# Kernel tuning notes

Hardware: AMD Instinct MI355X
Metric: run time of the kernel (lower is better)

The kernel has to match this reference:

```python
import jax, jax.numpy as jnp
import numpy as np

B, N, D = 8, 1024, 768
H, HD = 12, 64


def setup_inputs() -> dict:
    key = jax.random.key(0)
    ks = jax.random.split(key, 9)
    return {
        "x": jax.random.normal(ks[0], (B, N, D), dtype=jnp.float32),
        "Wq": jax.random.normal(ks[1], (H, HD, HD), dtype=jnp.float32) * (HD ** -0.5),
        "Wk": jax.random.normal(ks[2], (H, HD, HD), dtype=jnp.float32) * (HD ** -0.5),
        "Wv": jax.random.normal(ks[3], (H, HD, HD), dtype=jnp.float32) * (HD ** -0.5),
        "bq": jax.random.normal(ks[4], (H, HD), dtype=jnp.float32) * 0.02,
        "bk": jax.random.normal(ks[5], (H, HD), dtype=jnp.float32) * 0.02,
        "bv": jax.random.normal(ks[6], (H, HD), dtype=jnp.float32) * 0.02,
        "Wo": jax.random.normal(ks[7], (D, D), dtype=jnp.float32) * (D ** -0.5),
        "bo": jnp.zeros((D,), dtype=jnp.float32),
    }


def reference(x, Wq, Wk, Wv, bq, bk, bv, Wo, bo):
    # x: [B, N, D]; split into H heads of size HD along the feature dim
    b, n, d = x.shape
    h, hd = Wq.shape[0], Wq.shape[1]
    xh = x.reshape(b, n, h, hd)
    # per-head linear projections (stacked nn.Linear(head_dim, head_dim))
    q = jnp.einsum('bnhd,hde->bhne', xh, Wq) + bq[None, :, None, :]
    k = jnp.einsum('bnhd,hde->bhne', xh, Wk) + bk[None, :, None, :]
    v = jnp.einsum('bnhd,hde->bhne', xh, Wv) + bv[None, :, None, :]
    # NOTE: faithful quirk - scale uses FULL dim, not head_dim
    scale = d ** -0.5
    scores = jnp.einsum('bhid,bhjd->bhij', q, k) * scale  # [B,H,N,N]
    attn = jax.nn.softmax(scores, axis=-1)
    out = jnp.einsum('bhij,bhjd->bhid', attn, v)  # [B,H,N,HD]
    out = out.transpose(0, 2, 1, 3).reshape(b, n, d)  # concat heads
    return out @ Wo.T + bo  # wO: nn.Linear(dim, dim)
```

## Files before the change

kernel.cpp:

```cpp
#include <hip/hip_runtime.h>


typedef __attribute__((ext_vector_type(8))) short short8;
typedef __attribute__((ext_vector_type(4))) float floatx4;

#define MFMA16(a, b, c) __builtin_amdgcn_mfma_f32_16x16x32_bf16((a), (b), (c), 0, 0, 0)

#if __has_builtin(__builtin_amdgcn_exp2f)
#define EXP2(x) __builtin_amdgcn_exp2f(x)
#else
#define EXP2(x) __expf(0.6931471805599453f * (x))
#endif
#if __has_builtin(__builtin_amdgcn_rcpf)
#define RCP(x) __builtin_amdgcn_rcpf(x)
#else
#define RCP(x) (1.0f / (x))
#endif

__device__ __forceinline__ unsigned short f2bf(float f) {
    union { float f; unsigned int i; } c;
    c.f = f;
    unsigned int i = c.i;
    return (unsigned short)((i + 0x7fffu + ((i >> 16) & 1u)) >> 16);
}
__device__ __forceinline__ unsigned short f2bf_trunc(float f) {
    union { float f; unsigned int i; } c;
    c.f = f;
    return (unsigned short)(c.i >> 16);
}

__global__ __launch_bounds__(256) void prep_weights(
    const float* __restrict__ Wq, const float* __restrict__ Wk,
    const float* __restrict__ Wv, const float* __restrict__ Wo,
    unsigned short* __restrict__ Wqt, unsigned short* __restrict__ Wkt,
    unsigned short* __restrict__ Wvt, unsigned short* __restrict__ Wob)
{
    int tid = blockIdx.x * 256 + threadIdx.x;
    if (tid < 49152) {
        int h = tid >> 12, r = tid & 4095;
        int e = r >> 6, k = r & 63;
        int src = h * 4096 + k * 64 + e, dst = h * 4096 + e * 64 + k;
        Wqt[dst] = f2bf(Wq[src]);
        Wkt[dst] = f2bf(Wk[src]);
        Wvt[dst] = f2bf(Wv[src]);
    }
    for (int i = tid; i < 589824; i += 147456) Wob[i] = f2bf(Wo[i]);
}

__global__ __launch_bounds__(256) void qkv_proj(
    const float* __restrict__ x,
    const unsigned short* __restrict__ Wqt, const unsigned short* __restrict__ Wkt,
    const unsigned short* __restrict__ Wvt,
    const float* __restrict__ bq, const float* __restrict__ bk,
    const float* __restrict__ bv,
    unsigned short* __restrict__ Q, unsigned short* __restrict__ K,
    unsigned short* __restrict__ Vt)
{
    __shared__ __align__(16) unsigned short xlds[64 * 72];
    __shared__ __align__(16) unsigned short vlds[64 * 72];

    const int bh = blockIdx.y;
    const int b = bh / 12, h = bh % 12;
    const int wave = threadIdx.x >> 6, lane = threadIdx.x & 63;
    const int lrow = lane & 15, quad = lane >> 4;
    const int row0 = blockIdx.x * 64;
    const float scale = 0.052058776672f;

    {
        const int tr = threadIdx.x >> 2;
        const int tc = threadIdx.x & 3;
        const float* src = x + ((size_t)(b * 1024 + row0 + tr)) * 768
                           + h * 64 + tc * 16;
        float4 f0 = *(const float4*)(src);
        float4 f1 = *(const float4*)(src + 4);
        float4 f2 = *(const float4*)(src + 8);
        float4 f3 = *(const float4*)(src + 12);
        short8 p0, p1;
        p0[0] = (short)f2bf(f0.x); p0[1] = (short)f2bf(f0.y);
        p0[2] = (short)f2bf(f0.z); p0[3] = (short)f2bf(f0.w);
        p0[4] = (short)f2bf(f1.x); p0[5] = (short)f2bf(f1.y);
        p0[6] = (short)f2bf(f1.z); p0[7] = (short)f2bf(f1.w);
        p1[0] = (short)f2bf(f2.x); p1[1] = (short)f2bf(f2.y);
        p1[2] = (short)f2bf(f2.z); p1[3] = (short)f2bf(f2.w);
        p1[4] = (short)f2bf(f3.x); p1[5] = (short)f2bf(f3.y);
        p1[6] = (short)f2bf(f3.z); p1[7] = (short)f2bf(f3.w);
        *(short8*)&xlds[tr * 72 + tc * 16] = p0;
        *(short8*)&xlds[tr * 72 + tc * 16 + 8] = p1;
    }
    __syncthreads();

    short8 xb0 = *(const short8*)&xlds[(wave * 16 + lrow) * 72 + quad * 8];
    short8 xb1 = *(const short8*)&xlds[(wave * 16 + lrow) * 72 + 32 + quad * 8];

    const floatx4 zero = { 0.f, 0.f, 0.f, 0.f };

    const unsigned short* Wm[2] = { Wqt + h * 4096, Wkt + h * 4096 };
    const float* bm[2] = { bq + h * 64, bk + h * 64 };
    unsigned short* Om[2] = {
        Q + ((size_t)bh * 1024 + row0 + wave * 16 + lrow) * 64,
        K + ((size_t)bh * 1024 + row0 + wave * 16 + lrow) * 64 };
    #pragma unroll
    for (int m = 0; m < 2; ++m) {
        const unsigned short* W = Wm[m];
        #pragma unroll
        for (int t = 0; t < 4; ++t) {
            short8 wa0 = *(const short8*)(W + (t * 16 + lrow) * 64 + quad * 8);
            short8 wa1 = *(const short8*)(W + (t * 16 + lrow) * 64 + 32 + quad * 8);
            floatx4 acc = zero;
            acc = MFMA16(wa0, xb0, acc);
            acc = MFMA16(wa1, xb1, acc);
            float4 bias = *(const float4*)(bm[m] + t * 16 + quad * 4);
            const float bs[4] = { bias.x, bias.y, bias.z, bias.w };
            unsigned short pkd[4];
            #pragma unroll
            for (int r = 0; r < 4; ++r) {
                float v = acc[r] + bs[r];
                if (m == 0) v *= scale;
                pkd[r] = f2bf(v);
            }
            *(uint2*)(Om[m] + t * 16 + quad * 4) = *(uint2*)pkd;
        }
    }

    {
        const unsigned short* W = Wvt + h * 4096;
        const float* bvh = bv + h * 64;
        #pragma unroll
        for (int t = 0; t < 4; ++t) {
            short8 wa0 = *(const short8*)(W + (t * 16 + lrow) * 64 + quad * 8);
            short8 wa1 = *(const short8*)(W + (t * 16 + lrow) * 64 + 32 + quad * 8);
            floatx4 acc = zero;
            acc = MFMA16(wa0, xb0, acc);
            acc = MFMA16(wa1, xb1, acc);
            float4 bias = *(const float4*)(bvh + t * 16 + quad * 4);
            const float bs[4] = { bias.x, bias.y, bias.z, bias.w };
            #pragma unroll
            for (int r = 0; r < 4; ++r)
                vlds[(t * 16 + quad * 4 + r) * 72 + wave * 16 + lrow]
                    = f2bf(acc[r] + bs[r]);
        }
    }
    __syncthreads();
    {
        const int er = threadIdx.x >> 2;
        const int sc = threadIdx.x & 3;
        short8 v0 = *(const short8*)&vlds[er * 72 + sc * 16];
        short8 v1 = *(const short8*)&vlds[er * 72 + sc * 16 + 8];
        unsigned short* dst = Vt + (size_t)bh * 65536 + (size_t)er * 1024
                              + row0 + sc * 16;
        *(short8*)dst = v0;
        *(short8*)(dst + 8) = v1;
    }
}

__global__ __launch_bounds__(256) void attn_kernel(
    const unsigned short* __restrict__ Q, const unsigned short* __restrict__ K,
    const unsigned short* __restrict__ Vt, unsigned short* __restrict__ AO)
{
    __shared__ __align__(16) unsigned short Klds[64 * 72];
    __shared__ __align__(16) unsigned short Vlds[64 * 72];

    const int id = blockIdx.x + 16 * blockIdx.y;
    const int bh = (id & 7) * 12 + ((id % 96) >> 3);
    const int qb = id / 96;
    const int b = bh / 12, h = bh % 12;
    const int wave = threadIdx.x >> 6, lane = threadIdx.x & 63;
    const int lrow = lane & 15, quad = lane >> 4;
    const int qrow0 = qb * 64 + wave * 16;

    const unsigned short* Qb = Q + (size_t)bh * 65536;
    const unsigned short* Kb = K + (size_t)bh * 65536;
    const unsigned short* Vb = Vt + (size_t)bh * 65536;

    const int tch = threadIdx.x & 7, trow = threadIdx.x >> 3;

    short8 aq0, aq1;
    {
        const unsigned short* qr = Qb + (size_t)(qrow0 + lrow) * 64;
        aq0 = *(const short8*)(qr + quad * 8);
        aq1 = *(const short8*)(qr + 32 + quad * 8);
    }

    const int krow_base = ((lrow >> 2) * 8) + (lrow & 3);

    const floatx4 zero = { 0.f, 0.f, 0.f, 0.f };
    float part = 0.f;
    floatx4 Oacc[4];
    #pragma unroll
    for (int t = 0; t < 4; ++t) Oacc[t] = zero;

    for (int jt = 0; jt < 16; ++jt) {
        const int j0 = jt * 64;

        #pragma unroll
        for (int rr = 0; rr < 2; ++rr) {
            int r = trow + rr * 32;
            *(short8*)&Klds[r * 72 + tch * 8] =
                *(const short8*)(Kb + (size_t)(j0 + r) * 64 + tch * 8);
            *(short8*)&Vlds[r * 72 + tch * 8] =
                *(const short8*)(Vb + (size_t)r * 1024 + j0 + tch * 8);
        }
        __syncthreads();

        #pragma unroll
        for (int w = 0; w < 2; ++w) {
            short8 kA[2][2];
            #pragma unroll
            for (int tau = 0; tau < 2; ++tau) {
                int kr = w * 32 + krow_base + 4 * tau;
                kA[tau][0] = *(const short8*)&Klds[kr * 72 + quad * 8];
                kA[tau][1] = *(const short8*)&Klds[kr * 72 + 32 + quad * 8];
            }
            short8 vA[4];
            #pragma unroll
            for (int t = 0; t < 4; ++t)
                vA[t] = *(const short8*)&Vlds[(t * 16 + lrow) * 72
                                              + w * 32 + quad * 8];

            floatx4 s0 = zero, s1 = zero;
            s0 = MFMA16(kA[0][0], aq0, s0);
            s0 = MFMA16(kA[0][1], aq1, s0);
            s1 = MFMA16(kA[1][0], aq0, s1);
            s1 = MFMA16(kA[1][1], aq1, s1);

            short8 pk;
            #pragma unroll
            for (int r = 0; r < 4; ++r) {
                float p0 = EXP2(s0[r]);
                float p1 = EXP2(s1[r]);
                part += p0 + p1;
                pk[r] = (short)f2bf_trunc(p0);
                pk[4 + r] = (short)f2bf_trunc(p1);
            }
            #pragma unroll
            for (int t = 0; t < 4; ++t)
                Oacc[t] = MFMA16(vA[t], pk, Oacc[t]);
        }
        __syncthreads();
    }

    float ts = part;
    ts += __shfl_xor(ts, 16);
    ts += __shfl_xor(ts, 32);
    float inv = RCP(ts);
    unsigned short* orow = AO
        + ((size_t)(b * 1024 + qrow0 + lrow)) * 768 + h * 64;
    #pragma unroll
    for (int t = 0; t < 4; ++t) {
        unsigned short pkd[4];
        #pragma unroll
        for (int r = 0; r < 4; ++r)
            pkd[r] = f2bf(Oacc[t][r] * inv);
        *(uint2*)(orow + t * 16 + quad * 4) = *(uint2*)pkd;
    }
}

__global__ __launch_bounds__(256) void out_proj(
    const unsigned short* __restrict__ AO, const unsigned short* __restrict__ Wob,
    const float* __restrict__ bo, float* __restrict__ Y)
{
    __shared__ __align__(16) unsigned short Alds[128 * 40];
    __shared__ __align__(16) unsigned short Blds[64 * 40];

    const int wave = threadIdx.x >> 6, lane = threadIdx.x & 63;
    const int lrow = lane & 15, quad = lane >> 4;
    const int row0 = blockIdx.x * 128;
    const int c0 = blockIdx.y * 64;
    const int wrow = (wave >> 1) * 64, wcol = (wave & 1) * 32;

    const int tch = threadIdx.x & 3, trow = threadIdx.x >> 2;

    const floatx4 zero = { 0.f, 0.f, 0.f, 0.f };
    floatx4 acc[2][4];
    #pragma unroll
    for (int u = 0; u < 2; ++u)
        #pragma unroll
        for (int t = 0; t < 4; ++t) acc[u][t] = zero;

    for (int k0 = 0; k0 < 768; k0 += 32) {
        #pragma unroll
        for (int rr = 0; rr < 2; ++rr) {
            int r = trow + rr * 64;
            *(short8*)&Alds[r * 40 + tch * 8] =
                *(const short8*)(AO + (size_t)(row0 + r) * 768 + k0 + tch * 8);
        }
        *(short8*)&Blds[trow * 40 + tch * 8] =
            *(const short8*)(Wob + (size_t)(c0 + trow) * 768 + k0 + tch * 8);
        __syncthreads();

        short8 aoF[4], wF[2];
        #pragma unroll
        for (int t = 0; t < 4; ++t)
            aoF[t] = *(const short8*)&Alds[(wrow + t * 16 + lrow) * 40 + quad * 8];
        #pragma unroll
        for (int u = 0; u < 2; ++u)
            wF[u] = *(const short8*)&Blds[(wcol + u * 16 + lrow) * 40 + quad * 8];

        #pragma unroll
        for (int u = 0; u < 2; ++u)
            #pragma unroll
            for (int t = 0; t < 4; ++t)
                acc[u][t] = MFMA16(wF[u], aoF[t], acc[u][t]);
        __syncthreads();
    }

    #pragma unroll
    for (int u = 0; u < 2; ++u) {
        const int cb = c0 + wcol + u * 16 + quad * 4;
        float4 bias = *(const float4*)(bo + cb);
        const float bs[4] = { bias.x, bias.y, bias.z, bias.w };
        #pragma unroll
        for (int t = 0; t < 4; ++t) {
            const int row = row0 + wrow + t * 16 + lrow;
            float out[4];
            #pragma unroll
            for (int r = 0; r < 4; ++r) out[r] = acc[u][t][r] + bs[r];
            *(float4*)(Y + (size_t)row * 768 + cb) = *(float4*)out;
        }
    }
}

extern "C" void kernel_launch(void* const* d_in, const int* in_sizes, int n_in,
                              void* d_out, int out_size, void* d_ws, size_t ws_size,
                              hipStream_t stream)
{
    const float* x  = (const float*)d_in[0];
    const float* Wq = (const float*)d_in[1];
    const float* Wk = (const float*)d_in[2];
    const float* Wv = (const float*)d_in[3];
    const float* bq = (const float*)d_in[4];
    const float* bk = (const float*)d_in[5];
    const float* bv = (const float*)d_in[6];
    const float* Wo = (const float*)d_in[7];
    const float* bo = (const float*)d_in[8];

    unsigned short* Q   = (unsigned short*)d_ws;
    unsigned short* K   = Q + 6291456;
    unsigned short* Vt  = K + 6291456;
    unsigned short* AO  = Vt + 6291456;
    unsigned short* Wqt = AO + 6291456;
    unsigned short* Wkt = Wqt + 49152;
    unsigned short* Wvt = Wkt + 49152;
    unsigned short* Wob = Wvt + 49152;
    float* Y = (float*)d_out;

    prep_weights<<<dim3(576), 256, 0, stream>>>(Wq, Wk, Wv, Wo, Wqt, Wkt, Wvt, Wob);
    qkv_proj<<<dim3(16, 96), 256, 0, stream>>>(x, Wqt, Wkt, Wvt, bq, bk, bv, Q, K, Vt);
    attn_kernel<<<dim3(16, 96), 256, 0, stream>>>(Q, K, Vt, AO);
    out_proj<<<dim3(64, 12), 256, 0, stream>>>(AO, Wob, bo, Y);
}
```

Before: 176.7 us.

## Process two query sub-tiles per wave and register-prefetch next K/V tile

Each attention block now covers 128 query rows, with every wave handling two 16-row sub-tiles. This halves the grid and reuses each K/V tile loaded into LDS for twice as many queries. The next K/V tile is prefetched into registers while the current tile is computed, so global load latency overlaps with MFMA work. K rows are permuted on the store into LDS to keep the expected score column order. The costs are higher register pressure and fewer blocks, which may reduce occupancy.

```diff
diff --git a/kernel.cpp b/kernel.cpp
--- a/kernel.cpp
+++ b/kernel.cpp
@@ -160,54 +160,63 @@
     __shared__ __align__(16) unsigned short Klds[64 * 72];
     __shared__ __align__(16) unsigned short Vlds[64 * 72];
 
-    const int id = blockIdx.x + 16 * blockIdx.y;
-    const int bh = (id & 7) * 12 + ((id % 96) >> 3);
-    const int qb = id / 96;
+    const int bh = (int)blockIdx.x + ((int)blockIdx.y >> 3) * 8;
+    const int qb = blockIdx.y & 7;
     const int b = bh / 12, h = bh % 12;
     const int wave = threadIdx.x >> 6, lane = threadIdx.x & 63;
     const int lrow = lane & 15, quad = lane >> 4;
-    const int qrow0 = qb * 64 + wave * 16;
+    const int qrow0 = qb * 128 + wave * 32;
 
     const unsigned short* Qb = Q + (size_t)bh * 65536;
     const unsigned short* Kb = K + (size_t)bh * 65536;
     const unsigned short* Vb = Vt + (size_t)bh * 65536;
 
     const int tch = threadIdx.x & 7, trow = threadIdx.x >> 3;
-
-    short8 aq0, aq1;
-    {
-        const unsigned short* qr = Qb + (size_t)(qrow0 + lrow) * 64;
-        aq0 = *(const short8*)(qr + quad * 8);
-        aq1 = *(const short8*)(qr + 32 + quad * 8);
-    }
-
-    const int krow_base = ((lrow >> 2) * 8) + (lrow & 3);
+    const int slot0 = ((trow & 4) << 2) | ((trow >> 3) << 2) | (trow & 3);
+
+    short8 aq[2][2];
+    #pragma unroll
+    for (int mm = 0; mm < 2; ++mm) {
+        const unsigned short* qr = Qb + (size_t)(qrow0 + mm * 16 + lrow) * 64;
+        aq[mm][0] = *(const short8*)(qr + quad * 8);
+        aq[mm][1] = *(const short8*)(qr + 32 + quad * 8);
+    }
 
     const floatx4 zero = { 0.f, 0.f, 0.f, 0.f };
-    float part = 0.f;
-    floatx4 Oacc[4];
-    #pragma unroll
-    for (int t = 0; t < 4; ++t) Oacc[t] = zero;
+    float part[2] = { 0.f, 0.f };
+    floatx4 Oacc[2][4];
+    #pragma unroll
+    for (int mm = 0; mm < 2; ++mm)
+        #pragma unroll
+        for (int t = 0; t < 4; ++t) Oacc[mm][t] = zero;
+
+    short8 kpre[2], vpre[2];
+    kpre[0] = *(const short8*)(Kb + (size_t)trow * 64 + tch * 8);
+    kpre[1] = *(const short8*)(Kb + (size_t)(trow + 32) * 64 + tch * 8);
+    vpre[0] = *(const short8*)(Vb + (size_t)trow * 1024 + tch * 8);
+    vpre[1] = *(const short8*)(Vb + (size_t)(trow + 32) * 1024 + tch * 8);
 
     for (int jt = 0; jt < 16; ++jt) {
-        const int j0 = jt * 64;
-
-        #pragma unroll
-        for (int rr = 0; rr < 2; ++rr) {
-            int r = trow + rr * 32;
-            *(short8*)&Klds[r * 72 + tch * 8] =
-                *(const short8*)(Kb + (size_t)(j0 + r) * 64 + tch * 8);
-            *(short8*)&Vlds[r * 72 + tch * 8] =
-                *(const short8*)(Vb + (size_t)r * 1024 + j0 + tch * 8);
-        }
+        *(short8*)&Klds[slot0 * 72 + tch * 8] = kpre[0];
+        *(short8*)&Klds[(slot0 + 32) * 72 + tch * 8] = kpre[1];
+        *(short8*)&Vlds[trow * 72 + tch * 8] = vpre[0];
+        *(short8*)&Vlds[(trow + 32) * 72 + tch * 8] = vpre[1];
         __syncthreads();
+
+        {
+            const int jn = ((jt + 1) & 15) * 64;
+            kpre[0] = *(const short8*)(Kb + (size_t)(jn + trow) * 64 + tch * 8);
+            kpre[1] = *(const short8*)(Kb + (size_t)(jn + trow + 32) * 64 + tch * 8);
+            vpre[0] = *(const short8*)(Vb + (size_t)trow * 1024 + jn + tch * 8);
+            vpre[1] = *(const short8*)(Vb + (size_t)(trow + 32) * 1024 + jn + tch * 8);
+        }
 
         #pragma unroll
         for (int w = 0; w < 2; ++w) {
             short8 kA[2][2];
             #pragma unroll
             for (int tau = 0; tau < 2; ++tau) {
-                int kr = w * 32 + krow_base + 4 * tau;
+                int kr = w * 32 + tau * 16 + lrow;
                 kA[tau][0] = *(const short8*)&Klds[kr * 72 + quad * 8];
                 kA[tau][1] = *(const short8*)&Klds[kr * 72 + 32 + quad * 8];
             }
@@ -217,41 +226,47 @@
                 vA[t] = *(const short8*)&Vlds[(t * 16 + lrow) * 72
                                               + w * 32 + quad * 8];
 
-            floatx4 s0 = zero, s1 = zero;
-            s0 = MFMA16(kA[0][0], aq0, s0);
-            s0 = MFMA16(kA[0][1], aq1, s0);
-            s1 = MFMA16(kA[1][0], aq0, s1);
-            s1 = MFMA16(kA[1][1], aq1, s1);
-
-            short8 pk;
-            #pragma unroll
-            for (int r = 0; r < 4; ++r) {
-                float p0 = EXP2(s0[r]);
-                float p1 = EXP2(s1[r]);
-                part += p0 + p1;
-                pk[r] = (short)f2bf_trunc(p0);
-                pk[4 + r] = (short)f2bf_trunc(p1);
+            #pragma unroll
+            for (int mm = 0; mm < 2; ++mm) {
+                floatx4 s0 = zero, s1 = zero;
+                s0 = MFMA16(kA[0][0], aq[mm][0], s0);
+                s0 = MFMA16(kA[0][1], aq[mm][1], s0);
+                s1 = MFMA16(kA[1][0], aq[mm][0], s1);
+                s1 = MFMA16(kA[1][1], aq[mm][1], s1);
+
+                short8 pk;
+                #pragma unroll
+                for (int r = 0; r < 4; ++r) {
+                    float p0 = EXP2(s0[r]);
+                    float p1 = EXP2(s1[r]);
+                    part[mm] += p0 + p1;
+                    pk[r] = (short)f2bf_trunc(p0);
+                    pk[4 + r] = (short)f2bf_trunc(p1);
+                }
+                #pragma unroll
+                for (int t = 0; t < 4; ++t)
+                    Oacc[mm][t] = MFMA16(vA[t], pk, Oacc[mm][t]);
             }
-            #pragma unroll
-            for (int t = 0; t < 4; ++t)
-                Oacc[t] = MFMA16(vA[t], pk, Oacc[t]);
         }
         __syncthreads();
     }
 
-    float ts = part;
-    ts += __shfl_xor(ts, 16);
-    ts += __shfl_xor(ts, 32);
-    float inv = RCP(ts);
-    unsigned short* orow = AO
-        + ((size_t)(b * 1024 + qrow0 + lrow)) * 768 + h * 64;
-    #pragma unroll
-    for (int t = 0; t < 4; ++t) {
-        unsigned short pkd[4];
-        #pragma unroll
-        for (int r = 0; r < 4; ++r)
-            pkd[r] = f2bf(Oacc[t][r] * inv);
-        *(uint2*)(orow + t * 16 + quad * 4) = *(uint2*)pkd;
+    #pragma unroll
+    for (int mm = 0; mm < 2; ++mm) {
+        float ts = part[mm];
+        ts += __shfl_xor(ts, 16);
+        ts += __shfl_xor(ts, 32);
+        float inv = RCP(ts);
+        unsigned short* orow = AO
+            + ((size_t)(b * 1024 + qrow0 + mm * 16 + lrow)) * 768 + h * 64;
+        #pragma unroll
+        for (int t = 0; t < 4; ++t) {
+            unsigned short pkd[4];
+            #pragma unroll
+            for (int r = 0; r < 4; ++r)
+                pkd[r] = f2bf(Oacc[mm][t][r] * inv);
+            *(uint2*)(orow + t * 16 + quad * 4) = *(uint2*)pkd;
+        }
     }
 }
 
@@ -346,6 +361,6 @@
 
     prep_weights<<<dim3(576), 256, 0, stream>>>(Wq, Wk, Wv, Wo, Wqt, Wkt, Wvt, Wob);
     qkv_proj<<<dim3(16, 96), 256, 0, stream>>>(x, Wqt, Wkt, Wvt, bq, bk, bv, Q, K, Vt);
-    attn_kernel<<<dim3(16, 96), 256, 0, stream>>>(Q, K, Vt, AO);
+    attn_kernel<<<dim3(8, 96), 256, 0, stream>>>(Q, K, Vt, AO);
     out_proj<<<dim3(64, 12), 256, 0, stream>>>(AO, Wob, bo, Y);
 }
```

Result: no change. 173.4 us (-1.9%).
